# Performance work log

Hardware: AMD Instinct MI355X
Metric: run time of the kernel (lower is better)

Reference implementation:

```python
import jax, jax.numpy as jnp
import numpy as np

V, D, T, L, H = 32000, 1024, 2048, 2, 16
HS = D // H  # per-head dim (head_size // nheads)
FF = 4 * D
EPS = 1e-5


def _ln(x, g, b):
    m = jnp.mean(x, axis=-1, keepdims=True)
    v = jnp.mean((x - m) ** 2, axis=-1, keepdims=True)
    return (x - m) * jax.lax.rsqrt(v + EPS) * g + b


def setup_inputs() -> dict:
    key = jax.random.key(0)
    ks = jax.random.split(key, 16)
    s = lambda k, shape, fan: jax.random.normal(k, shape, jnp.float32) * (fan ** -0.5)
    return {
        "inputs": jax.random.randint(ks[0], (1, T), 0, V, dtype=jnp.int64),
        "tok_emb": s(ks[1], (V, D), D),
        "pos_emb": s(ks[2], (T, D), D),
        "ln1_g": jnp.ones((L, D)), "ln1_b": jnp.zeros((L, D)),
        "wq": s(ks[3], (L, H, D, HS), D),
        "wk": s(ks[4], (L, H, D, HS), D),
        "wv": s(ks[5], (L, H, D, HS), D),
        "ln2_g": jnp.ones((L, D)), "ln2_b": jnp.zeros((L, D)),
        "w1": s(ks[6], (L, D, FF), D), "b1": jnp.zeros((L, FF)),
        "w2": s(ks[7], (L, FF, D), FF), "b2": jnp.zeros((L, D)),
        "lnf_g": jnp.ones((D,)), "lnf_b": jnp.zeros((D,)),
        "w_un": s(ks[8], (D, V), D), "b_un": jnp.zeros((V,)),
    }


def reference(inputs, tok_emb, pos_emb, ln1_g, ln1_b, wq, wk, wv,
              ln2_g, ln2_b, w1, b1, w2, b2, lnf_g, lnf_b, w_un, b_un):
    b, t = inputs.shape
    x = tok_emb[inputs] + pos_emb[:t]  # [B,T,D]
    mask = jnp.tril(jnp.ones((t, t), dtype=bool))
    scale = jnp.asarray(D, x.dtype) ** -0.5  # source scales by x.shape[-1]**-0.5
    neg_inf = jnp.asarray(-jnp.inf, x.dtype)
    for l in range(L):
        h = _ln(x, ln1_g[l], ln1_b[l])
        q = jnp.einsum('btc,hcs->bhts', h, wq[l])
        k = jnp.einsum('btc,hcs->bhts', h, wk[l])
        v = jnp.einsum('btc,hcs->bhts', h, wv[l])
        scores = jnp.einsum('bhts,bhus->bhtu', q, k) * scale  # [B,H,T,T]
        scores = jnp.where(mask, scores, neg_inf)
        p = jax.nn.softmax(scores, axis=-1)
        att = jnp.einsum('bhtu,bhus->bhts', p, v)  # [B,H,T,HS]
        att = att.transpose(0, 2, 1, 3).reshape(b, t, H * HS)
        x = x + att
        h = _ln(x, ln2_g[l], ln2_b[l])
        h = jax.nn.relu(h @ w1[l] + b1[l]) @ w2[l] + b2[l]
        x = x + h
    x = _ln(x, lnf_g, lnf_b)
    return x @ w_un + b_un  # [B,T,V]
```

## Files before the change

kernel.cpp:

```cpp
#include <hip/hip_runtime.h>
#include <hip/hip_bf16.h>

#define TT 2048
#define DD 1024
#define NH 16
#define HSZ 64
#define FFD 4096
#define VV 32000
#define NL 2

typedef __bf16 bf16x8 __attribute__((ext_vector_type(8)));
typedef float f32x4 __attribute__((ext_vector_type(4)));

__device__ __forceinline__ unsigned short f2bf(float f) {
    unsigned int u = __float_as_uint(f);
    return (unsigned short)((u + 0x7FFFu + ((u >> 16) & 1u)) >> 16);
}

#define GLL(gsrc, ldst) \
  __builtin_amdgcn_global_load_lds((const __attribute__((address_space(1))) void*)(gsrc), \
                                   (__attribute__((address_space(3))) void*)(ldst), 16, 0, 0)

#define SWZ64(L)  ((L) ^ ((((L) >> 7) & 3) << 4))
#define SWZ128(L) ((L) ^ ((((L) >> 7) & 7) << 4))

__global__ __launch_bounds__(256) void embed_kernel(
    const int* __restrict__ idx, const float* __restrict__ tok,
    const float* __restrict__ pos, float* __restrict__ x)
{
    int t = blockIdx.x;
    int d4 = threadIdx.x * 4;
    int token = idx[t];
    float4 a = *(const float4*)&tok[(size_t)token * DD + d4];
    float4 p = *(const float4*)&pos[(size_t)t * DD + d4];
    float4 r;
    r.x = a.x + p.x; r.y = a.y + p.y; r.z = a.z + p.z; r.w = a.w + p.w;
    *(float4*)&x[(size_t)t * DD + d4] = r;
}

__global__ __launch_bounds__(256) void ln_kernel(
    const float* __restrict__ x, const float* __restrict__ g,
    const float* __restrict__ b, unsigned short* __restrict__ out)
{
    int t = blockIdx.x;
    int tid = threadIdx.x;
    int d4 = tid * 4;
    float4 xv = *(const float4*)&x[(size_t)t * DD + d4];
    float s  = xv.x + xv.y + xv.z + xv.w;
    float s2 = xv.x*xv.x + xv.y*xv.y + xv.z*xv.z + xv.w*xv.w;
    #pragma unroll
    for (int off = 32; off >= 1; off >>= 1) {
        s  += __shfl_xor(s,  off);
        s2 += __shfl_xor(s2, off);
    }
    __shared__ float ls[4], ls2[4];
    int w = tid >> 6;
    if ((tid & 63) == 0) { ls[w] = s; ls2[w] = s2; }
    __syncthreads();
    float sum  = ls[0] + ls[1] + ls[2] + ls[3];
    float sum2 = ls2[0] + ls2[1] + ls2[2] + ls2[3];
    float mean = sum * (1.0f / DD);
    float var  = sum2 * (1.0f / DD) - mean * mean;
    float r = rsqrtf(var + 1e-5f);
    float4 gv = *(const float4*)&g[d4];
    float4 bv = *(const float4*)&b[d4];
    ushort4 pk;
    pk.x = f2bf((xv.x - mean) * r * gv.x + bv.x);
    pk.y = f2bf((xv.y - mean) * r * gv.y + bv.y);
    pk.z = f2bf((xv.z - mean) * r * gv.z + bv.z);
    pk.w = f2bf((xv.w - mean) * r * gv.w + bv.w);
    *(ushort4*)&out[(size_t)t * DD + d4] = pk;
}

__global__ __launch_bounds__(256) void tcast(
    const float* __restrict__ src, unsigned short* __restrict__ dst,
    int R, int C, size_t sstride, size_t dstride)
{
    __shared__ float tile[64][65];
    const float* s = src + (size_t)blockIdx.z * sstride;
    unsigned short* d = dst + (size_t)blockIdx.z * dstride;
    int c0 = blockIdx.x * 64, r0 = blockIdx.y * 64;
    #pragma unroll
    for (int i = 0; i < 16; ++i) {
        int id = i * 256 + threadIdx.x;
        int rr = id >> 6, cc = id & 63;
        tile[rr][cc] = s[(size_t)(r0 + rr) * C + (c0 + cc)];
    }
    __syncthreads();
    #pragma unroll
    for (int i = 0; i < 16; ++i) {
        int id = i * 256 + threadIdx.x;
        int cc = id >> 6, rr = id & 63;
        d[(size_t)(c0 + cc) * R + (r0 + rr)] = f2bf(tile[rr][cc]);
    }
}

__global__ __launch_bounds__(256) void qkv_tcast(
    const float* __restrict__ wq, const float* __restrict__ wk,
    const float* __restrict__ wv, unsigned short* __restrict__ dst)
{
    __shared__ float tile[64][65];
    int l = blockIdx.z;
    int mat = blockIdx.y >> 4, hh = blockIdx.y & 15;
    const float* s = (mat == 0) ? wq : (mat == 1) ? wk : wv;
    s += (((size_t)l * NH + hh) * DD) * HSZ;
    int r0 = blockIdx.x * 64;
    #pragma unroll
    for (int i = 0; i < 16; ++i) {
        int id = i * 256 + threadIdx.x;
        int rr = id >> 6, cc = id & 63;
        tile[rr][cc] = s[(size_t)(r0 + rr) * HSZ + cc];
    }
    __syncthreads();
    unsigned short* d = dst + (size_t)l * 3072 * DD + ((size_t)mat * DD + hh * HSZ) * DD;
    #pragma unroll
    for (int i = 0; i < 16; ++i) {
        int id = i * 256 + threadIdx.x;
        int cc = id >> 6, rr = id & 63;
        d[(size_t)cc * DD + (r0 + rr)] = f2bf(tile[rr][cc]);
    }
}

template<int EPI>
__global__ __launch_bounds__(256) void mgemm(
    const unsigned short* __restrict__ A, const unsigned short* __restrict__ Bt,
    const float* __restrict__ bias, void* __restrict__ outp,
    int M, int N, int K)
{
    __shared__ unsigned short As[2][128 * 32];
    __shared__ unsigned short Bs[2][128 * 32];
    int tid = threadIdx.x;
    int w = tid >> 6, lane = tid & 63;
    int l15 = lane & 15, l4 = lane >> 4;
    int bm = blockIdx.y * 128, bn = blockIdx.x * 128;
    int wr = (w >> 1) * 64, wc = (w & 1) * 64;

    f32x4 zz = {0.f, 0.f, 0.f, 0.f};
    f32x4 acc[4][4];
    #pragma unroll
    for (int m = 0; m < 4; ++m)
        #pragma unroll
        for (int n = 0; n < 4; ++n) acc[m][n] = zz;

    int t16 = tid * 16;
    int lg = SWZ64(t16);
    int srow = lg >> 6;
    int skel = (lg & 63) >> 1;
    const unsigned short* aS0 = A + (size_t)(bm + srow) * K + skel;
    const unsigned short* aS1 = A + (size_t)(bm + 64 + srow) * K + skel;
    const unsigned short* bS0 = Bt + (size_t)(bn + srow) * K + skel;
    const unsigned short* bS1 = Bt + (size_t)(bn + 64 + srow) * K + skel;

    #define STAGE(t, buf) do { int kk_ = (t) * 32; \
        GLL(aS0 + kk_, (char*)As[buf] + w * 1024); \
        GLL(aS1 + kk_, (char*)As[buf] + 4096 + w * 1024); \
        GLL(bS0 + kk_, (char*)Bs[buf] + w * 1024); \
        GLL(bS1 + kk_, (char*)Bs[buf] + 4096 + w * 1024); } while (0)

    int aoff[4], boff[4];
    #pragma unroll
    for (int m = 0; m < 4; ++m) {
        int la = (wr + m * 16 + l15) * 64 + l4 * 16;
        aoff[m] = SWZ64(la);
        int lb = (wc + m * 16 + l15) * 64 + l4 * 16;
        boff[m] = SWZ64(lb);
    }

    int nt = K >> 5;
    STAGE(0, 0);
    STAGE(1, 1);
    for (int t = 0; t < nt; ++t) {
        int buf = t & 1;
        if (t + 1 < nt) asm volatile("s_waitcnt vmcnt(4)" ::: "memory");
        else            asm volatile("s_waitcnt vmcnt(0)" ::: "memory");
        __builtin_amdgcn_sched_barrier(0);
        __builtin_amdgcn_s_barrier();
        __builtin_amdgcn_sched_barrier(0);
        bf16x8 af[4], bfr[4];
        #pragma unroll
        for (int m = 0; m < 4; ++m) af[m] = *(const bf16x8*)((const char*)As[buf] + aoff[m]);
        #pragma unroll
        for (int n = 0; n < 4; ++n) bfr[n] = *(const bf16x8*)((const char*)Bs[buf] + boff[n]);
        #pragma unroll
        for (int m = 0; m < 4; ++m)
            #pragma unroll
            for (int n = 0; n < 4; ++n)
                acc[m][n] = __builtin_amdgcn_mfma_f32_16x16x32_bf16(af[m], bfr[n], acc[m][n], 0, 0, 0);
        __builtin_amdgcn_sched_barrier(0);
        __builtin_amdgcn_s_barrier();
        __builtin_amdgcn_sched_barrier(0);
        if (t + 2 < nt) STAGE(t + 2, buf);
    }
    #undef STAGE

    #pragma unroll
    for (int m = 0; m < 4; ++m) {
        int row0 = bm + wr + m * 16 + l4 * 4;
        #pragma unroll
        for (int n = 0; n < 4; ++n) {
            int col = bn + wc + n * 16 + l15;
            f32x4 v = acc[m][n];
            if (EPI == 0) {
                int mat = col >> 10, hh = (col >> 6) & 15, ss = col & 63;
                unsigned short* base = (unsigned short*)outp + (size_t)mat * ((size_t)NH * TT * HSZ);
                if (mat < 2) {
                    #pragma unroll
                    for (int i = 0; i < 4; ++i)
                        base[((size_t)hh * TT + row0 + i) * HSZ + ss] = f2bf(v[i]);
                } else {
                    ushort4 pk;
                    pk.x = f2bf(v[0]); pk.y = f2bf(v[1]); pk.z = f2bf(v[2]); pk.w = f2bf(v[3]);
                    *(ushort4*)&base[((size_t)hh * HSZ + ss) * TT + row0] = pk;
                }
            } else if (EPI == 1) {
                float bb = bias[col];
                unsigned short* o = (unsigned short*)outp;
                #pragma unroll
                for (int i = 0; i < 4; ++i)
                    o[(size_t)(row0 + i) * FFD + col] = f2bf(fmaxf(v[i] + bb, 0.f));
            } else if (EPI == 2) {
                float bb = bias[col];
                float* xx = (float*)outp;
                #pragma unroll
                for (int i = 0; i < 4; ++i)
                    xx[(size_t)(row0 + i) * DD + col] += v[i] + bb;
            }
        }
    }
}

__global__ __launch_bounds__(512, 2) void mgemm256(
    const unsigned short* __restrict__ A, const unsigned short* __restrict__ Bt,
    const float* __restrict__ bias, float* __restrict__ outp,
    int M, int N, int K)
{
    __shared__ unsigned short As[2][2][128 * 64];
    __shared__ unsigned short Bs[2][2][128 * 64];
    int tid = threadIdx.x;
    int w = tid >> 6, lane = tid & 63;
    int l15 = lane & 15, l4 = lane >> 4;
    int wr = w >> 2, wc = w & 3;
    int bid = blockIdx.x;
    int xcd = bid & 7, j = bid >> 3;
    int mt = j & 7, p = xcd * 16 + (j >> 3);
    if (p >= N / 256) return;
    int bm = mt * 256, bn = p * 256;

    f32x4 zz = {0.f, 0.f, 0.f, 0.f};
    f32x4 acc[8][4];
    #pragma unroll
    for (int m = 0; m < 8; ++m)
        #pragma unroll
        for (int n = 0; n < 4; ++n) acc[m][n] = zz;

    int L0 = w * 1024 + lane * 16;
    int Ls = SWZ128(L0);
    int srow = Ls >> 7;
    int skel = (Ls & 127) >> 1;
    const unsigned short* aS[2], *bS[2];
    aS[0] = A + (size_t)(bm + srow) * K + skel;
    aS[1] = A + (size_t)(bm + 128 + srow) * K + skel;
    bS[0] = Bt + (size_t)(bn + srow) * K + skel;
    bS[1] = Bt + (size_t)(bn + 128 + srow) * K + skel;
    size_t g1 = (size_t)64 * K;

    #define STAGE6(t, buf) do { int kk_ = (t) * 64; \
        GLL(aS[0] + kk_,      (char*)As[buf][0] + w * 1024); \
        GLL(aS[0] + g1 + kk_, (char*)As[buf][0] + 8192 + w * 1024); \
        GLL(aS[1] + kk_,      (char*)As[buf][1] + w * 1024); \
        GLL(aS[1] + g1 + kk_, (char*)As[buf][1] + 8192 + w * 1024); \
        GLL(bS[0] + kk_,      (char*)Bs[buf][0] + w * 1024); \
        GLL(bS[0] + g1 + kk_, (char*)Bs[buf][0] + 8192 + w * 1024); \
        GLL(bS[1] + kk_,      (char*)Bs[buf][1] + w * 1024); \
        GLL(bS[1] + g1 + kk_, (char*)Bs[buf][1] + 8192 + w * 1024); } while (0)

    int aoff[8][2], boff[4][2];
    #pragma unroll
    for (int m = 0; m < 8; ++m)
        #pragma unroll
        for (int ks = 0; ks < 2; ++ks) {
            int La = (m * 16 + l15) * 128 + ks * 64 + l4 * 16;
            aoff[m][ks] = SWZ128(La);
        }
    #pragma unroll
    for (int n = 0; n < 4; ++n)
        #pragma unroll
        for (int ks = 0; ks < 2; ++ks) {
            int Lb = ((wc & 1) * 64 + n * 16 + l15) * 128 + ks * 64 + l4 * 16;
            boff[n][ks] = SWZ128(Lb);
        }

    int nt = K >> 6;
    STAGE6(0, 0);
    STAGE6(1, 1);
    for (int t = 0; t < nt; ++t) {
        int buf = t & 1;
        if (t + 1 < nt) asm volatile("s_waitcnt vmcnt(8)" ::: "memory");
        else            asm volatile("s_waitcnt vmcnt(0)" ::: "memory");
        __builtin_amdgcn_sched_barrier(0);
        __builtin_amdgcn_s_barrier();
        __builtin_amdgcn_sched_barrier(0);
        const char* ab = (const char*)As[buf][wr];
        const char* bb = (const char*)Bs[buf][wc >> 1];
        bf16x8 bfr[4][2];
        #pragma unroll
        for (int n = 0; n < 4; ++n)
            #pragma unroll
            for (int ks = 0; ks < 2; ++ks)
                bfr[n][ks] = *(const bf16x8*)(bb + boff[n][ks]);
        __builtin_amdgcn_s_setprio(1);
        #pragma unroll
        for (int rh = 0; rh < 2; ++rh) {
            bf16x8 af[4][2];
            #pragma unroll
            for (int mm = 0; mm < 4; ++mm)
                #pragma unroll
                for (int ks = 0; ks < 2; ++ks)
                    af[mm][ks] = *(const bf16x8*)(ab + aoff[rh * 4 + mm][ks]);
            #pragma unroll
            for (int mm = 0; mm < 4; ++mm)
                #pragma unroll
                for (int n = 0; n < 4; ++n) {
                    acc[rh*4+mm][n] = __builtin_amdgcn_mfma_f32_16x16x32_bf16(af[mm][0], bfr[n][0], acc[rh*4+mm][n], 0, 0, 0);
                    acc[rh*4+mm][n] = __builtin_amdgcn_mfma_f32_16x16x32_bf16(af[mm][1], bfr[n][1], acc[rh*4+mm][n], 0, 0, 0);
                }
        }
        __builtin_amdgcn_s_setprio(0);
        __builtin_amdgcn_sched_barrier(0);
        __builtin_amdgcn_s_barrier();
        __builtin_amdgcn_sched_barrier(0);
        if (t + 2 < nt) STAGE6(t + 2, buf);
    }
    #undef STAGE6

    #pragma unroll
    for (int m = 0; m < 8; ++m) {
        int row0 = bm + wr * 128 + m * 16 + l4 * 4;
        #pragma unroll
        for (int n = 0; n < 4; ++n) {
            int col = bn + wc * 64 + n * 16 + l15;
            float bb = bias[col];
            f32x4 v = acc[m][n];
            #pragma unroll
            for (int i = 0; i < 4; ++i)
                outp[(size_t)(row0 + i) * VV + col] = v[i] + bb;
        }
    }
}

__global__ __launch_bounds__(256) void attn_kernel(
    const unsigned short* __restrict__ qg, const unsigned short* __restrict__ kg,
    const unsigned short* __restrict__ vt, float* __restrict__ x)
{
    __shared__ unsigned short Ks[2][64 * 64];
    __shared__ unsigned short Vs[2][64 * 64];
    __shared__ unsigned short Ps[4][16 * 64];
    int tid = threadIdx.x;
    int w = tid >> 6, lane = tid & 63;
    int l15 = lane & 15, l4 = lane >> 4;
    int hh = blockIdx.y;
    int qb = blockIdx.x * 64;

    const unsigned short* qrow = qg + ((size_t)hh * TT + qb + w * 16 + l15) * HSZ + l4 * 8;
    bf16x8 qf0 = *(const bf16x8*)(qrow);
    bf16x8 qf1 = *(const bf16x8*)(qrow + 32);

    int t16 = tid * 16;
    int lgs = SWZ128(t16);
    int surow = lgs >> 7;
    int subyte = lgs & 127;
    const char* kbase = (const char*)(kg + (size_t)hh * TT * HSZ);
    const char* vbase = (const char*)(vt + (size_t)hh * HSZ * TT);

    #define ASTAGE(ib, buf) do { \
        int ub_ = (ib) * 64; \
        GLL(kbase + (size_t)(ub_ + surow) * 128 + subyte,          (char*)Ks[buf] + w * 1024); \
        GLL(kbase + (size_t)(ub_ + 32 + surow) * 128 + subyte,     (char*)Ks[buf] + 4096 + w * 1024); \
        GLL(vbase + (size_t)surow * 4096 + ub_ * 2 + subyte,       (char*)Vs[buf] + w * 1024); \
        GLL(vbase + (size_t)(surow + 32) * 4096 + ub_ * 2 + subyte,(char*)Vs[buf] + 4096 + w * 1024); \
    } while (0)

    f32x4 zz = {0.f, 0.f, 0.f, 0.f};
    f32x4 o[4];
    float mrun[4], lrun[4];
    #pragma unroll
    for (int i = 0; i < 4; ++i) { o[i] = zz; mrun[i] = -INFINITY; lrun[i] = 0.f; }

    const float scale = 0.03125f;
    int nkv = (qb >> 6) + 1;
    ASTAGE(0, 0);
    __syncthreads();
    int cur = 0;
    for (int ib = 0; ib < nkv; ++ib) {
        int ub = ib * 64;
        bool diag = (ub == qb);
        if (ib + 1 < nkv) ASTAGE(ib + 1, cur ^ 1);
        const char* ksc = (const char*)Ks[cur];
        const char* vsc = (const char*)Vs[cur];

        f32x4 sfr[4];
        #pragma unroll
        for (int f = 0; f < 4; ++f) {
            int lgb = (f * 16 + l15) * 128 + l4 * 16;
            bf16x8 b0 = *(const bf16x8*)(ksc + SWZ128(lgb));
            bf16x8 b1 = *(const bf16x8*)(ksc + SWZ128(lgb + 64));
            f32x4 z = zz;
            z = __builtin_amdgcn_mfma_f32_16x16x32_bf16(qf0, b0, z, 0, 0, 0);
            z = __builtin_amdgcn_mfma_f32_16x16x32_bf16(qf1, b1, z, 0, 0, 0);
            sfr[f] = z;
        }
        #pragma unroll
        for (int f = 0; f < 4; ++f)
            #pragma unroll
            for (int i = 0; i < 4; ++i) {
                float s = sfr[f][i] * scale;
                if (diag && (f * 16 + l15) > (w * 16 + l4 * 4 + i)) s = -INFINITY;
                sfr[f][i] = s;
            }
        #pragma unroll
        for (int i = 0; i < 4; ++i) {
            float t = fmaxf(fmaxf(sfr[0][i], sfr[1][i]), fmaxf(sfr[2][i], sfr[3][i]));
            t = fmaxf(t, __shfl_xor(t, 1));
            t = fmaxf(t, __shfl_xor(t, 2));
            t = fmaxf(t, __shfl_xor(t, 4));
            t = fmaxf(t, __shfl_xor(t, 8));
            float mn = fmaxf(mrun[i], t);
            float c = __expf(mrun[i] - mn);
            mrun[i] = mn;
            float ps = 0.f;
            #pragma unroll
            for (int f = 0; f < 4; ++f) {
                float p = __expf(sfr[f][i] - mn);
                sfr[f][i] = p;
                ps += p;
            }
            ps += __shfl_xor(ps, 1); ps += __shfl_xor(ps, 2);
            ps += __shfl_xor(ps, 4); ps += __shfl_xor(ps, 8);
            lrun[i] = lrun[i] * c + ps;
            #pragma unroll
            for (int sf = 0; sf < 4; ++sf) o[sf][i] *= c;
        }
        unsigned short* pw = Ps[w];
        #pragma unroll
        for (int i = 0; i < 4; ++i) {
            int q = l4 * 4 + i;
            #pragma unroll
            for (int f = 0; f < 4; ++f) {
                int lgb = q * 128 + (f * 16 + l15) * 2;
                *(unsigned short*)((char*)pw + SWZ128(lgb)) = f2bf(sfr[f][i]);
            }
        }
        bf16x8 pa0 = *(const bf16x8*)((const char*)pw + SWZ128(l15 * 128 + l4 * 16));
        bf16x8 pa1 = *(const bf16x8*)((const char*)pw + SWZ128(l15 * 128 + 64 + l4 * 16));
        #pragma unroll
        for (int sf = 0; sf < 4; ++sf) {
            int lgb = (sf * 16 + l15) * 128 + l4 * 16;
            bf16x8 v0 = *(const bf16x8*)(vsc + SWZ128(lgb));
            bf16x8 v1 = *(const bf16x8*)(vsc + SWZ128(lgb + 64));
            o[sf] = __builtin_amdgcn_mfma_f32_16x16x32_bf16(pa0, v0, o[sf], 0, 0, 0);
            o[sf] = __builtin_amdgcn_mfma_f32_16x16x32_bf16(pa1, v1, o[sf], 0, 0, 0);
        }
        __syncthreads();
        cur ^= 1;
    }
    #undef ASTAGE
    float rl[4];
    #pragma unroll
    for (int i = 0; i < 4; ++i) rl[i] = 1.0f / lrun[i];
    #pragma unroll
    for (int sf = 0; sf < 4; ++sf)
        #pragma unroll
        for (int i = 0; i < 4; ++i) {
            int q = qb + w * 16 + l4 * 4 + i;
            int d = hh * HSZ + sf * 16 + l15;
            x[(size_t)q * DD + d] += o[sf][i] * rl[i];
        }
}

extern "C" void kernel_launch(void* const* d_in, const int* in_sizes, int n_in,
                              void* d_out, int out_size, void* d_ws, size_t ws_size,
                              hipStream_t stream)
{
    const int*   idx    = (const int*)  d_in[0];
    const float* tok    = (const float*)d_in[1];
    const float* pos    = (const float*)d_in[2];
    const float* ln1_g  = (const float*)d_in[3];
    const float* ln1_b  = (const float*)d_in[4];
    const float* wq     = (const float*)d_in[5];
    const float* wk     = (const float*)d_in[6];
    const float* wv     = (const float*)d_in[7];
    const float* ln2_g  = (const float*)d_in[8];
    const float* ln2_b  = (const float*)d_in[9];
    const float* w1     = (const float*)d_in[10];
    const float* b1     = (const float*)d_in[11];
    const float* w2     = (const float*)d_in[12];
    const float* b2     = (const float*)d_in[13];
    const float* lnf_g  = (const float*)d_in[14];
    const float* lnf_b  = (const float*)d_in[15];
    const float* w_un   = (const float*)d_in[16];
    const float* b_un   = (const float*)d_in[17];
    float* out = (float*)d_out;

    char* W = (char*)d_ws;
    float*          x    = (float*)(W);
    unsigned short* h    = (unsigned short*)(W + 8388608);
    unsigned short* qg   = (unsigned short*)(W + 12582912);
    unsigned short* kg   = (unsigned short*)(W + 16777216);
    unsigned short* vt   = (unsigned short*)(W + 20971520);
    unsigned short* h1   = (unsigned short*)(W + 25165824);
    unsigned short* wqkvT= (unsigned short*)(W + 41943040);
    unsigned short* w1T  = (unsigned short*)(W + 54525952);
    unsigned short* w2T  = (unsigned short*)(W + 71303168);
    unsigned short* wunT = (unsigned short*)(W + 88080384);
    (void)kg; (void)ws_size; (void)in_sizes; (void)n_in; (void)out_size;

    qkv_tcast<<<dim3(16, 48, 2), 256, 0, stream>>>(wq, wk, wv, wqkvT);
    tcast<<<dim3(64, 16, 2), 256, 0, stream>>>(w1, w1T, DD, FFD, (size_t)DD * FFD, (size_t)DD * FFD);
    tcast<<<dim3(16, 64, 2), 256, 0, stream>>>(w2, w2T, FFD, DD, (size_t)FFD * DD, (size_t)FFD * DD);
    tcast<<<dim3(500, 16, 1), 256, 0, stream>>>(w_un, wunT, DD, VV, 0, 0);

    embed_kernel<<<TT, 256, 0, stream>>>(idx, tok, pos, x);

    for (int l = 0; l < NL; ++l) {
        ln_kernel<<<TT, 256, 0, stream>>>(x, ln1_g + l * DD, ln1_b + l * DD, h);
        mgemm<0><<<dim3(24, 16), 256, 0, stream>>>(h, wqkvT + (size_t)l * 3072 * DD, nullptr, qg, TT, 3072, DD);
        attn_kernel<<<dim3(32, 16), 256, 0, stream>>>(qg, kg, vt, x);
        ln_kernel<<<TT, 256, 0, stream>>>(x, ln2_g + l * DD, ln2_b + l * DD, h);
        mgemm<1><<<dim3(32, 16), 256, 0, stream>>>(h, w1T + (size_t)l * FFD * DD, b1 + (size_t)l * FFD, h1, TT, FFD, DD);
        mgemm<2><<<dim3(8, 16), 256, 0, stream>>>(h1, w2T + (size_t)l * DD * FFD, b2 + (size_t)l * DD, x, TT, DD, FFD);
    }

    ln_kernel<<<TT, 256, 0, stream>>>(x, lnf_g, lnf_b, h);
    mgemm256<<<dim3(1024), 512, 0, stream>>>(h, wunT, b_un, out, TT, VV, DD);
}
```

Measured before the change: 733.2 us.

## Transpose QK^T MFMA so softmax row stats reduce across fewer lanes

Swaps the MFMA operands for the score computation so each lane holds one query row's scores. The row max and sum then need only two cross-lane shuffles instead of four per row, and the P tile is written to LDS with packed 32-bit stores instead of scattered 16-bit ones. The per-row rescale factors and the final normaliser are fetched back into the O layout with shuffles. It also raises wave priority around the MFMA blocks with s_setprio to favour matrix issue. The cost is extra shuffles for the correction factors and a reworked causal mask that must match the new layout.

```diff
diff --git a/kernel.cpp b/kernel.cpp
--- a/kernel.cpp
+++ b/kernel.cpp
@@ -382,9 +382,9 @@
 
     f32x4 zz = {0.f, 0.f, 0.f, 0.f};
     f32x4 o[4];
-    float mrun[4], lrun[4];
-    #pragma unroll
-    for (int i = 0; i < 4; ++i) { o[i] = zz; mrun[i] = -INFINITY; lrun[i] = 0.f; }
+    #pragma unroll
+    for (int i = 0; i < 4; ++i) o[i] = zz;
+    float mrun = -INFINITY, lrun = 0.f;
 
     const float scale = 0.03125f;
     int nkv = (qb >> 6) + 1;
@@ -399,59 +399,65 @@
         const char* vsc = (const char*)Vs[cur];
 
         f32x4 sfr[4];
+        __builtin_amdgcn_s_setprio(1);
         #pragma unroll
         for (int f = 0; f < 4; ++f) {
             int lgb = (f * 16 + l15) * 128 + l4 * 16;
-            bf16x8 b0 = *(const bf16x8*)(ksc + SWZ128(lgb));
-            bf16x8 b1 = *(const bf16x8*)(ksc + SWZ128(lgb + 64));
+            bf16x8 k0 = *(const bf16x8*)(ksc + SWZ128(lgb));
+            bf16x8 k1 = *(const bf16x8*)(ksc + SWZ128(lgb + 64));
             f32x4 z = zz;
-            z = __builtin_amdgcn_mfma_f32_16x16x32_bf16(qf0, b0, z, 0, 0, 0);
-            z = __builtin_amdgcn_mfma_f32_16x16x32_bf16(qf1, b1, z, 0, 0, 0);
+            z = __builtin_amdgcn_mfma_f32_16x16x32_bf16(k0, qf0, z, 0, 0, 0);
+            z = __builtin_amdgcn_mfma_f32_16x16x32_bf16(k1, qf1, z, 0, 0, 0);
             sfr[f] = z;
         }
+        __builtin_amdgcn_s_setprio(0);
+
+        float mx = -INFINITY;
         #pragma unroll
         for (int f = 0; f < 4; ++f)
             #pragma unroll
             for (int i = 0; i < 4; ++i) {
                 float s = sfr[f][i] * scale;
-                if (diag && (f * 16 + l15) > (w * 16 + l4 * 4 + i)) s = -INFINITY;
+                if (diag && (16 * f + (l4 << 2) + i) > (w * 16 + l15)) s = -INFINITY;
                 sfr[f][i] = s;
+                mx = fmaxf(mx, s);
             }
-        #pragma unroll
-        for (int i = 0; i < 4; ++i) {
-            float t = fmaxf(fmaxf(sfr[0][i], sfr[1][i]), fmaxf(sfr[2][i], sfr[3][i]));
-            t = fmaxf(t, __shfl_xor(t, 1));
-            t = fmaxf(t, __shfl_xor(t, 2));
-            t = fmaxf(t, __shfl_xor(t, 4));
-            t = fmaxf(t, __shfl_xor(t, 8));
-            float mn = fmaxf(mrun[i], t);
-            float c = __expf(mrun[i] - mn);
-            mrun[i] = mn;
-            float ps = 0.f;
-            #pragma unroll
-            for (int f = 0; f < 4; ++f) {
+        mx = fmaxf(mx, __shfl_xor(mx, 16));
+        mx = fmaxf(mx, __shfl_xor(mx, 32));
+        float mn = fmaxf(mrun, mx);
+        float c = __expf(mrun - mn);
+        mrun = mn;
+        float ps = 0.f;
+        #pragma unroll
+        for (int f = 0; f < 4; ++f)
+            #pragma unroll
+            for (int i = 0; i < 4; ++i) {
                 float p = __expf(sfr[f][i] - mn);
                 sfr[f][i] = p;
                 ps += p;
             }
-            ps += __shfl_xor(ps, 1); ps += __shfl_xor(ps, 2);
-            ps += __shfl_xor(ps, 4); ps += __shfl_xor(ps, 8);
-            lrun[i] = lrun[i] * c + ps;
-            #pragma unroll
-            for (int sf = 0; sf < 4; ++sf) o[sf][i] *= c;
-        }
+        ps += __shfl_xor(ps, 16);
+        ps += __shfl_xor(ps, 32);
+        lrun = lrun * c + ps;
+        #pragma unroll
+        for (int i = 0; i < 4; ++i) {
+            float ci = __shfl(c, (lane & 48) + (l4 << 2) + i);
+            #pragma unroll
+            for (int sf = 0; sf < 4; ++sf) o[sf][i] *= ci;
+        }
+
         unsigned short* pw = Ps[w];
         #pragma unroll
-        for (int i = 0; i < 4; ++i) {
-            int q = l4 * 4 + i;
-            #pragma unroll
-            for (int f = 0; f < 4; ++f) {
-                int lgb = q * 128 + (f * 16 + l15) * 2;
-                *(unsigned short*)((char*)pw + SWZ128(lgb)) = f2bf(sfr[f][i]);
-            }
+        for (int f = 0; f < 4; ++f) {
+            unsigned a0 = ((unsigned)f2bf(sfr[f][0])) | (((unsigned)f2bf(sfr[f][1])) << 16);
+            unsigned a1 = ((unsigned)f2bf(sfr[f][2])) | (((unsigned)f2bf(sfr[f][3])) << 16);
+            int byte0 = l15 * 128 + (16 * f + (l4 << 2)) * 2;
+            *(unsigned*)((char*)pw + SWZ128(byte0)) = a0;
+            *(unsigned*)((char*)pw + SWZ128(byte0 + 4)) = a1;
         }
         bf16x8 pa0 = *(const bf16x8*)((const char*)pw + SWZ128(l15 * 128 + l4 * 16));
         bf16x8 pa1 = *(const bf16x8*)((const char*)pw + SWZ128(l15 * 128 + 64 + l4 * 16));
+        __builtin_amdgcn_s_setprio(1);
         #pragma unroll
         for (int sf = 0; sf < 4; ++sf) {
             int lgb = (sf * 16 + l15) * 128 + l4 * 16;
@@ -460,13 +466,15 @@
             o[sf] = __builtin_amdgcn_mfma_f32_16x16x32_bf16(pa0, v0, o[sf], 0, 0, 0);
             o[sf] = __builtin_amdgcn_mfma_f32_16x16x32_bf16(pa1, v1, o[sf], 0, 0, 0);
         }
+        __builtin_amdgcn_s_setprio(0);
         __syncthreads();
         cur ^= 1;
     }
     #undef ASTAGE
     float rl[4];
     #pragma unroll
-    for (int i = 0; i < 4; ++i) rl[i] = 1.0f / lrun[i];
+    for (int i = 0; i < 4; ++i)
+        rl[i] = 1.0f / __shfl(lrun, (lane & 48) + (l4 << 2) + i);
     #pragma unroll
     for (int sf = 0; sf < 4; ++sf)
         #pragma unroll
```

After: 702.2 us. -4.2%, faster.
